# Optimization experiments

Measured on AMD Instinct MI355X. Metric: run time of the kernel, lower is better.

Reference implementation:

```python
import jax, jax.numpy as jnp
import numpy as np

T, B, D_IN, D_HID, D_OUT = 256, 128, 512, 1024, 512


def setup_inputs() -> dict:
    key = jax.random.key(0)
    ks = jax.random.split(key, 7)
    s_i = 1.0 / np.sqrt(D_IN)
    s_h = 1.0 / np.sqrt(D_HID)
    return {
        "x": jax.random.normal(ks[0], (T, B, D_IN), jnp.float32),
        "Wi": jax.random.normal(ks[1], (D_HID, D_IN), jnp.float32) * s_i,
        "bi": jax.random.normal(ks[2], (D_HID,), jnp.float32) * s_i,
        "Wh": jax.random.normal(ks[3], (D_HID, D_HID), jnp.float32) * s_h,
        "bh": jax.random.normal(ks[4], (D_HID,), jnp.float32) * s_h,
        "Wo": jax.random.normal(ks[5], (D_OUT, D_HID), jnp.float32) * s_h,
        "bo": jax.random.normal(ks[6], (D_OUT,), jnp.float32) * s_h,
    }


def reference(x, Wi, bi, Wh, bh, Wo, bo):
    # Elman RNN: h_t = relu(x_t @ Wi^T + bi + h_{t-1} @ Wh^T + bh)
    # Precompute input projection for all timesteps (one big GEMM).
    zi = jnp.einsum("tbi,hi->tbh", x, Wi) + bi  # [T,B,H]

    def step(h, zi_t):
        z = jax.nn.relu(zi_t + h @ Wh.T + bh)
        return z, z

    h0 = jnp.zeros((x.shape[1], Wh.shape[0]), x.dtype)
    _, hidden = jax.lax.scan(step, h0, zi)  # hidden: [T,B,H]

    y = jnp.einsum("tbh,oh->tbo", hidden, Wo) + bo  # [T,B,O]
    hT = hidden[-1][None]  # [1,B,H]
    return hidden, hT, y
```

## Files before the change

### kernel.cpp

```cpp
#include <hip/hip_runtime.h>
#include <hip/hip_bf16.h>
#include <type_traits>

#define T_ 256
#define B_ 128
#define DIN_ 512
#define H_ 1024
#define DOUT_ 512

typedef __attribute__((ext_vector_type(8))) short bf16x8;
typedef __attribute__((ext_vector_type(4))) short s16x4;
typedef __attribute__((ext_vector_type(4))) float f32x4;
typedef unsigned long long u64;

__device__ unsigned g_flags[2048];

__device__ inline short f2bf(float f) {
    return __builtin_bit_cast(short, __float2bfloat16(f));
}
__device__ inline float4 zload4(const short* p) {
    u64 u = *(const u64*)p;
    auto bf = [](unsigned x) { return __builtin_bit_cast(float, x << 16); };
    return make_float4(bf((unsigned)(u & 0xffff) ), bf((unsigned)((u >> 16) & 0xffff)),
                       bf((unsigned)((u >> 32) & 0xffff)), bf((unsigned)((u >> 48) & 0xffff)));
}
__device__ inline u64 pack4bf(float v0, float v1, float v2, float v3) {
    return (u64)(unsigned short)f2bf(v0)
         | ((u64)(unsigned short)f2bf(v1) << 16)
         | ((u64)(unsigned short)f2bf(v2) << 32)
         | ((u64)(unsigned short)f2bf(v3) << 48);
}

#define AT_LD64(p)     __hip_atomic_load((p), __ATOMIC_RELAXED, __HIP_MEMORY_SCOPE_AGENT)
#define AT_SWP64(p, v) (void)__hip_atomic_exchange((p), (v), __ATOMIC_RELAXED, __HIP_MEMORY_SCOPE_AGENT)
#define AT_LD32(p)     __hip_atomic_load((p), __ATOMIC_RELAXED, __HIP_MEMORY_SCOPE_AGENT)
#define AT_SWP32(p, v) (void)__hip_atomic_exchange((p), (v), __ATOMIC_RELAXED, __HIP_MEMORY_SCOPE_AGENT)

__global__ void zero_flags() { g_flags[blockIdx.x * 256 + threadIdx.x] = 0; }

template <typename OUT_T>
__global__ __launch_bounds__(256)
void gemm_bias(const float* __restrict__ A, const float* __restrict__ W,
               const float* __restrict__ b1, const float* __restrict__ b2,
               OUT_T* __restrict__ out, int M, int N, int K)
{
    __shared__ short lA[4096];
    __shared__ short lB[4096];
    const int ntiles = N >> 7;
    const int bm = blockIdx.x / ntiles;
    const int bn = blockIdx.x % ntiles;
    const size_t m0 = (size_t)bm << 7;
    const size_t n0 = (size_t)bn << 7;
    const int tid = threadIdx.x;
    const int w = tid >> 6, l = tid & 63;
    const int wm = (w >> 1) << 6, wn = (w & 1) << 6;

    f32x4 acc[4][4] = {};
    float4 ra[4], rb[4];

    auto load_regs = [&](int k0) {
#pragma unroll
        for (int i = 0; i < 4; ++i) {
            int s = i * 256 + tid;
            int row = s >> 3, kq = s & 7;
            ra[i] = *(const float4*)(A + (m0 + row) * K + k0 + kq * 4);
            rb[i] = *(const float4*)(W + (n0 + row) * K + k0 + kq * 4);
        }
    };
    auto store_lds = [&]() {
#pragma unroll
        for (int i = 0; i < 4; ++i) {
            int s = i * 256 + tid;
            int row = s >> 3, kq = s & 7;
            int off = ((row >> 4) * 64 + ((row & 15) | ((kq >> 1) << 4))) * 8 + (kq & 1) * 4;
            s16x4 pa = { f2bf(ra[i].x), f2bf(ra[i].y), f2bf(ra[i].z), f2bf(ra[i].w) };
            s16x4 pb = { f2bf(rb[i].x), f2bf(rb[i].y), f2bf(rb[i].z), f2bf(rb[i].w) };
            *(s16x4*)&lA[off] = pa;
            *(s16x4*)&lB[off] = pb;
        }
    };

    load_regs(0);
    const int KI = K >> 5;
    for (int ki = 0; ki < KI; ++ki) {
        __syncthreads();
        store_lds();
        __syncthreads();
        if (ki + 1 < KI) load_regs((ki + 1) << 5);
        bf16x8 aF[4], bF[4];
#pragma unroll
        for (int i = 0; i < 4; ++i) {
            aF[i] = *(const bf16x8*)&lA[(((wm >> 4) + i) * 64 + l) * 8];
            bF[i] = *(const bf16x8*)&lB[(((wn >> 4) + i) * 64 + l) * 8];
        }
#pragma unroll
        for (int i = 0; i < 4; ++i)
#pragma unroll
            for (int j = 0; j < 4; ++j)
                acc[i][j] = __builtin_amdgcn_mfma_f32_16x16x32_bf16(aF[i], bF[j], acc[i][j], 0, 0, 0);
    }

#pragma unroll
    for (int j = 0; j < 4; ++j) {
        const int col = (int)n0 + wn + j * 16 + (l & 15);
        float bb = b1[col];
        if (b2) bb += b2[col];
#pragma unroll
        for (int i = 0; i < 4; ++i) {
#pragma unroll
            for (int r = 0; r < 4; ++r) {
                int row = (int)m0 + wm + i * 16 + (l >> 4) * 4 + r;
                float v = acc[i][j][r] + bb;
                if constexpr (std::is_same<OUT_T, short>::value)
                    out[(size_t)row * N + col] = f2bf(v);
                else
                    out[(size_t)row * N + col] = v;
            }
        }
    }
}

__global__ __launch_bounds__(256, 1)
void rnn_rec6(const short* __restrict__ zi, const float* __restrict__ Wh,
              float* __restrict__ hidden, unsigned short* __restrict__ hbuf)
{
    const int wg = blockIdx.x;
    const int bg = wg >> 4, cg = wg & 15;
    const int tid = threadIdx.x, w = tid >> 6, l = tid & 63;
    const int b = l & 15, hi = l >> 4;
    const int ocw = cg * 64 + w * 16;

    __shared__ u64 lds_h[4096];

    bf16x8 wh[32];
#pragma unroll
    for (int kk = 0; kk < 32; ++kk) {
        const float* wp = Wh + (size_t)(ocw + b) * H_ + kk * 32 + hi * 8;
        float4 a = *(const float4*)wp;
        float4 c = *(const float4*)(wp + 4);
        bf16x8 v = { f2bf(a.x), f2bf(a.y), f2bf(a.z), f2bf(a.w),
                     f2bf(c.x), f2bf(c.y), f2bf(c.z), f2bf(c.w) };
        wh[kk] = v;
    }

    const int f0 = ocw + hi * 4;
    float4 z = zload4(zi + ((size_t)bg * 16 + b) * H_ + f0);

    const int kk2 = f0 >> 5, j0 = f0 & 7;
    const int lane2 = b | (((f0 >> 3) & 3) << 4);

#pragma unroll 1
    for (int t = 0; t < T_; ++t) {
        const size_t zb = (size_t)t * B_ * H_;
        f32x4 acc0 = {}, acc1 = {};
        if (t > 0) {
            const u64* hp = (const u64*)hbuf + (size_t)(((t + 1) & 1) * 8 + bg) * 4096;
            u64 sv[16];
#pragma unroll
            for (int i = 0; i < 16; ++i)
                sv[i] = AT_LD64(hp + i * 256 + tid);
#pragma unroll
            for (int i = 0; i < 16; ++i)
                lds_h[i * 256 + tid] = sv[i];
            __syncthreads();
#pragma unroll
            for (int kk = 0; kk < 32; ++kk) {
                bf16x8 hbf = *(const bf16x8*)&lds_h[(kk * 64 + l) * 2];
                if (kk & 1)
                    acc1 = __builtin_amdgcn_mfma_f32_16x16x32_bf16(wh[kk], hbf, acc1, 0, 0, 0);
                else
                    acc0 = __builtin_amdgcn_mfma_f32_16x16x32_bf16(wh[kk], hbf, acc0, 0, 0, 0);
            }
        }
        float v0 = fmaxf(acc0[0] + acc1[0] + z.x, 0.f);
        float v1 = fmaxf(acc0[1] + acc1[1] + z.y, 0.f);
        float v2 = fmaxf(acc0[2] + acc1[2] + z.z, 0.f);
        float v3 = fmaxf(acc0[3] + acc1[3] + z.w, 0.f);
        *(float4*)(hidden + zb + (size_t)(bg * 16 + b) * H_ + f0) =
            make_float4(v0, v1, v2, v3);
        unsigned short* hwS = hbuf + (size_t)((t & 1) * 8 + bg) * 16384;
        AT_SWP64((u64*)(hwS + (kk2 * 64 + lane2) * 8 + j0), pack4bf(v0, v1, v2, v3));

        __syncthreads();
        if (tid == 0)
            AT_SWP32(&g_flags[wg * 16], (unsigned)(t + 1));

        if (t + 1 < T_)
            z = zload4(zi + ((size_t)(t + 1) * B_ + bg * 16 + b) * H_ + f0);

        if (w == 0) {
            const unsigned tgt = (unsigned)(t + 1);
            const unsigned* fp = &g_flags[(bg * 16 + (l & 15)) * 16];
            unsigned v;
            do {
                v = AT_LD32(fp);
            } while (!__all((int)(v >= tgt)));
        }
        __syncthreads();
    }
}

__global__ __launch_bounds__(256)
void copy_k(const float4* __restrict__ s, float4* __restrict__ d)
{
    int i = blockIdx.x * 256 + threadIdx.x;
    d[i] = s[i];
}

extern "C" void kernel_launch(void* const* d_in, const int* in_sizes, int n_in,
                              void* d_out, int out_size, void* d_ws, size_t ws_size,
                              hipStream_t stream)
{
    const float* x  = (const float*)d_in[0];
    const float* Wi = (const float*)d_in[1];
    const float* bi = (const float*)d_in[2];
    const float* Wh = (const float*)d_in[3];
    const float* bh = (const float*)d_in[4];
    const float* Wo = (const float*)d_in[5];
    const float* bo = (const float*)d_in[6];

    float* hidden = (float*)d_out;
    float* hT     = hidden + (size_t)T_ * B_ * H_;
    float* y      = hT + (size_t)B_ * H_;

    const size_t HBUF_B = (size_t)2 * B_ * H_ * sizeof(short);
    const size_t ZI_B   = (size_t)T_ * B_ * H_ * sizeof(short);

    zero_flags<<<dim3(8), dim3(256), 0, stream>>>();

    short* zi;
    unsigned short* hbuf;
    if (ws_size >= HBUF_B + ZI_B) {
        hbuf = (unsigned short*)d_ws;
        zi   = (short*)((char*)d_ws + HBUF_B);
    } else {
        zi   = (short*)y;
        hbuf = (unsigned short*)hT;
    }

    gemm_bias<short><<<dim3(2048), dim3(256), 0, stream>>>(
        x, Wi, bi, bh, zi, T_ * B_, H_, DIN_);
    rnn_rec6<<<dim3(128), dim3(256), 0, stream>>>(zi, Wh, hidden, hbuf);

    copy_k<<<dim3(128), dim3(256), 0, stream>>>(
        (const float4*)(hidden + (size_t)(T_ - 1) * B_ * H_), (float4*)hT);

    gemm_bias<float><<<dim3(1024), dim3(256), 0, stream>>>(
        hidden, Wo, bo, nullptr, y, T_ * B_, DOUT_, H_);
}
```

Measured before the change: 846.8 us.

## Replace flag barrier with sign-bit epoch tags embedded in hidden-state payload

Removes the per-step global flag write and spin-wait barrier in the recurrent kernel. Each bf16 hidden value carries a phase tag in its sign bit, which is safe because post-ReLU values are non-negative. Consumers poll the data itself until all tags match the expected epoch, then clear the bits. This removes a barrier round trip per timestep, but relies on 64-bit atomic stores being seen as a unit and on the buffer's initial memset pattern differing from the first expected tag.

```diff
diff --git a/kernel.cpp b/kernel.cpp
--- a/kernel.cpp
+++ b/kernel.cpp
@@ -13,8 +13,6 @@
 typedef __attribute__((ext_vector_type(4))) float f32x4;
 typedef unsigned long long u64;
 
-__device__ unsigned g_flags[2048];
-
 __device__ inline short f2bf(float f) {
     return __builtin_bit_cast(short, __float2bfloat16(f));
 }
@@ -31,12 +29,8 @@
          | ((u64)(unsigned short)f2bf(v3) << 48);
 }
 
-#define AT_LD64(p)     __hip_atomic_load((p), __ATOMIC_RELAXED, __HIP_MEMORY_SCOPE_AGENT)
-#define AT_SWP64(p, v) (void)__hip_atomic_exchange((p), (v), __ATOMIC_RELAXED, __HIP_MEMORY_SCOPE_AGENT)
-#define AT_LD32(p)     __hip_atomic_load((p), __ATOMIC_RELAXED, __HIP_MEMORY_SCOPE_AGENT)
-#define AT_SWP32(p, v) (void)__hip_atomic_exchange((p), (v), __ATOMIC_RELAXED, __HIP_MEMORY_SCOPE_AGENT)
-
-__global__ void zero_flags() { g_flags[blockIdx.x * 256 + threadIdx.x] = 0; }
+#define AT_LD64(p)    __hip_atomic_load((p), __ATOMIC_RELAXED, __HIP_MEMORY_SCOPE_AGENT)
+#define AT_ST64(p, v) __hip_atomic_store((p), (v), __ATOMIC_RELAXED, __HIP_MEMORY_SCOPE_AGENT)
 
 template <typename OUT_T>
 __global__ __launch_bounds__(256)
@@ -121,7 +115,7 @@
 }
 
 __global__ __launch_bounds__(256, 1)
-void rnn_rec6(const short* __restrict__ zi, const float* __restrict__ Wh,
+void rnn_rec7(const short* __restrict__ zi, const float* __restrict__ Wh,
               float* __restrict__ hidden, unsigned short* __restrict__ hbuf)
 {
     const int wg = blockIdx.x;
@@ -129,6 +123,7 @@
     const int tid = threadIdx.x, w = tid >> 6, l = tid & 63;
     const int b = l & 15, hi = l >> 4;
     const int ocw = cg * 64 + w * 16;
+    const u64 SIGN = 0x8000800080008000ull;
 
     __shared__ u64 lds_h[4096];
 
@@ -154,11 +149,26 @@
         const size_t zb = (size_t)t * B_ * H_;
         f32x4 acc0 = {}, acc1 = {};
         if (t > 0) {
+            const u64 expmask = (((t - 1) >> 1) & 1) ? SIGN : 0ull;
             const u64* hp = (const u64*)hbuf + (size_t)(((t + 1) & 1) * 8 + bg) * 4096;
             u64 sv[16];
 #pragma unroll
             for (int i = 0; i < 16; ++i)
                 sv[i] = AT_LD64(hp + i * 256 + tid);
+            unsigned pend = 0xFFFFu;
+            while (pend) {
+#pragma unroll
+                for (int i = 0; i < 16; ++i) {
+                    if (pend & (1u << i)) {
+                        if ((sv[i] & SIGN) == expmask) pend &= ~(1u << i);
+                        else sv[i] = AT_LD64(hp + i * 256 + tid);
+                    }
+                }
+            }
+            if (expmask) {
+#pragma unroll
+                for (int i = 0; i < 16; ++i) sv[i] &= ~SIGN;
+            }
 #pragma unroll
             for (int i = 0; i < 16; ++i)
                 lds_h[i * 256 + tid] = sv[i];
@@ -179,23 +189,12 @@
         *(float4*)(hidden + zb + (size_t)(bg * 16 + b) * H_ + f0) =
             make_float4(v0, v1, v2, v3);
         unsigned short* hwS = hbuf + (size_t)((t & 1) * 8 + bg) * 16384;
-        AT_SWP64((u64*)(hwS + (kk2 * 64 + lane2) * 8 + j0), pack4bf(v0, v1, v2, v3));
-
-        __syncthreads();
-        if (tid == 0)
-            AT_SWP32(&g_flags[wg * 16], (unsigned)(t + 1));
+        u64 payload = pack4bf(v0, v1, v2, v3) | (((t >> 1) & 1) ? SIGN : 0ull);
+        AT_ST64((u64*)(hwS + (kk2 * 64 + lane2) * 8 + j0), payload);
 
         if (t + 1 < T_)
             z = zload4(zi + ((size_t)(t + 1) * B_ + bg * 16 + b) * H_ + f0);
 
-        if (w == 0) {
-            const unsigned tgt = (unsigned)(t + 1);
-            const unsigned* fp = &g_flags[(bg * 16 + (l & 15)) * 16];
-            unsigned v;
-            do {
-                v = AT_LD32(fp);
-            } while (!__all((int)(v >= tgt)));
-        }
         __syncthreads();
     }
 }
@@ -225,8 +224,6 @@
 
     const size_t HBUF_B = (size_t)2 * B_ * H_ * sizeof(short);
     const size_t ZI_B   = (size_t)T_ * B_ * H_ * sizeof(short);
-
-    zero_flags<<<dim3(8), dim3(256), 0, stream>>>();
 
     short* zi;
     unsigned short* hbuf;
@@ -238,9 +235,11 @@
         hbuf = (unsigned short*)hT;
     }
 
+    hipMemsetAsync(hbuf, 0xAA, HBUF_B, stream);
+
     gemm_bias<short><<<dim3(2048), dim3(256), 0, stream>>>(
         x, Wi, bi, bh, zi, T_ * B_, H_, DIN_);
-    rnn_rec6<<<dim3(128), dim3(256), 0, stream>>>(zi, Wh, hidden, hbuf);
+    rnn_rec7<<<dim3(128), dim3(256), 0, stream>>>(zi, Wh, hidden, hbuf);
 
     copy_k<<<dim3(128), dim3(256), 0, stream>>>(
         (const float4*)(hidden + (size_t)(T_ - 1) * B_ * H_), (float4*)hT);
```

Measured after the change: 1.033 ms. 22.0% more time.

## Speculatively prefetch hidden state with sign-bit epoch tags and per-wave flag counters

Applied to the files above, without the earlier changes.

The recurrent kernel now starts loading the next step's hidden-state buffer before the cross-workgroup flag wait. It tags each packed bf16 value with an epoch bit carried in the sign bits, which is safe because the values are post-ReLU and therefore non-negative. After the wait, only stale entries whose epoch bits do not match are reloaded. The per-workgroup __syncthreads plus a single flag store is replaced by a per-wave atomic add, and the wait target becomes four times the step. The goal is to hide global load latency behind the barrier wait and to remove a block-wide sync from the critical path. In exchange, the code relies on every sign bit being clear, and a stale-but-tagged-fresh read could occur when the double buffer is reused.

```diff
diff --git a/kernel.cpp b/kernel.cpp
--- a/kernel.cpp
+++ b/kernel.cpp
@@ -34,7 +34,7 @@
 #define AT_LD64(p)     __hip_atomic_load((p), __ATOMIC_RELAXED, __HIP_MEMORY_SCOPE_AGENT)
 #define AT_SWP64(p, v) (void)__hip_atomic_exchange((p), (v), __ATOMIC_RELAXED, __HIP_MEMORY_SCOPE_AGENT)
 #define AT_LD32(p)     __hip_atomic_load((p), __ATOMIC_RELAXED, __HIP_MEMORY_SCOPE_AGENT)
-#define AT_SWP32(p, v) (void)__hip_atomic_exchange((p), (v), __ATOMIC_RELAXED, __HIP_MEMORY_SCOPE_AGENT)
+#define AT_ADD32(p, v) (void)__hip_atomic_fetch_add((p), (v), __ATOMIC_RELAXED, __HIP_MEMORY_SCOPE_AGENT)
 
 __global__ void zero_flags() { g_flags[blockIdx.x * 256 + threadIdx.x] = 0; }
 
@@ -121,7 +121,7 @@
 }
 
 __global__ __launch_bounds__(256, 1)
-void rnn_rec6(const short* __restrict__ zi, const float* __restrict__ Wh,
+void rnn_rec9(const short* __restrict__ zi, const float* __restrict__ Wh,
               float* __restrict__ hidden, unsigned short* __restrict__ hbuf)
 {
     const int wg = blockIdx.x;
@@ -129,6 +129,7 @@
     const int tid = threadIdx.x, w = tid >> 6, l = tid & 63;
     const int b = l & 15, hi = l >> 4;
     const int ocw = cg * 64 + w * 16;
+    const u64 SIGN = 0x8000800080008000ull;
 
     __shared__ u64 lds_h[4096];
 
@@ -149,16 +150,29 @@
     const int kk2 = f0 >> 5, j0 = f0 & 7;
     const int lane2 = b | (((f0 >> 3) & 3) << 4);
 
+    u64 sv[16];
+
 #pragma unroll 1
     for (int t = 0; t < T_; ++t) {
         const size_t zb = (size_t)t * B_ * H_;
         f32x4 acc0 = {}, acc1 = {};
         if (t > 0) {
+            const u64 expmask = (((t - 1) >> 1) & 1) ? SIGN : 0ull;
             const u64* hp = (const u64*)hbuf + (size_t)(((t + 1) & 1) * 8 + bg) * 4096;
-            u64 sv[16];
-#pragma unroll
-            for (int i = 0; i < 16; ++i)
-                sv[i] = AT_LD64(hp + i * 256 + tid);
+            if (t >= 3) {
+#pragma unroll
+                for (int i = 0; i < 16; ++i)
+                    if ((sv[i] & SIGN) != expmask)
+                        sv[i] = AT_LD64(hp + i * 256 + tid);
+            } else {
+#pragma unroll
+                for (int i = 0; i < 16; ++i)
+                    sv[i] = AT_LD64(hp + i * 256 + tid);
+            }
+            if (expmask) {
+#pragma unroll
+                for (int i = 0; i < 16; ++i) sv[i] &= ~SIGN;
+            }
 #pragma unroll
             for (int i = 0; i < 16; ++i)
                 lds_h[i * 256 + tid] = sv[i];
@@ -179,22 +193,30 @@
         *(float4*)(hidden + zb + (size_t)(bg * 16 + b) * H_ + f0) =
             make_float4(v0, v1, v2, v3);
         unsigned short* hwS = hbuf + (size_t)((t & 1) * 8 + bg) * 16384;
-        AT_SWP64((u64*)(hwS + (kk2 * 64 + lane2) * 8 + j0), pack4bf(v0, v1, v2, v3));
-
-        __syncthreads();
-        if (tid == 0)
-            AT_SWP32(&g_flags[wg * 16], (unsigned)(t + 1));
-
-        if (t + 1 < T_)
+        u64 pay = pack4bf(v0, v1, v2, v3) | (((t >> 1) & 1) ? SIGN : 0ull);
+        AT_SWP64((u64*)(hwS + (kk2 * 64 + lane2) * 8 + j0), pay);
+
+        asm volatile("s_waitcnt vmcnt(0)" ::: "memory");
+        __builtin_amdgcn_sched_barrier(0);
+        if (l == 0)
+            AT_ADD32(&g_flags[(bg * 16 + cg) * 16], 1u);
+
+        if (t + 1 < T_) {
             z = zload4(zi + ((size_t)(t + 1) * B_ + bg * 16 + b) * H_ + f0);
-
-        if (w == 0) {
-            const unsigned tgt = (unsigned)(t + 1);
-            const unsigned* fp = &g_flags[(bg * 16 + (l & 15)) * 16];
-            unsigned v;
-            do {
-                v = AT_LD32(fp);
-            } while (!__all((int)(v >= tgt)));
+            if (t + 1 >= 3) {
+                const u64* hpn = (const u64*)hbuf + (size_t)((t & 1) * 8 + bg) * 4096;
+#pragma unroll
+                for (int i = 0; i < 16; ++i)
+                    sv[i] = AT_LD64(hpn + i * 256 + tid);
+            }
+            if (w == 0) {
+                const unsigned tgt = 4u * (unsigned)(t + 1);
+                const unsigned* fp = &g_flags[(bg * 16 + (l & 15)) * 16];
+                unsigned fv;
+                do {
+                    fv = AT_LD32(fp);
+                } while (!__all((int)(fv >= tgt)));
+            }
         }
         __syncthreads();
     }
@@ -240,7 +262,7 @@
 
     gemm_bias<short><<<dim3(2048), dim3(256), 0, stream>>>(
         x, Wi, bi, bh, zi, T_ * B_, H_, DIN_);
-    rnn_rec6<<<dim3(128), dim3(256), 0, stream>>>(zi, Wh, hidden, hbuf);
+    rnn_rec9<<<dim3(128), dim3(256), 0, stream>>>(zi, Wh, hidden, hbuf);
 
     copy_k<<<dim3(128), dim3(256), 0, stream>>>(
         (const float4*)(hidden + (size_t)(T_ - 1) * B_ * H_), (float4*)hT);
```

Measured after the change: 1.020 ms. 1.2x slower.
